# Performance work log

Measured on AMD Instinct MI355X. Metric: run time of the kernel, lower is better.

Reference implementation:

```python
import jax, jax.numpy as jnp
import numpy as np

N_ITER = 30       # fixed-point iterations (repo iterates to tol 3e-6, max 300)
POWER_ITERS = 50  # power iteration steps for spectral radius
KAPPA = 0.9
EPS = 1e-12


def project_l1_ball_rows(W, v):
    # projection_norm_inf: project each row of W onto the L1 ball of radius v
    a = jnp.abs(W)
    s = -jnp.sort(-a, axis=-1)                      # descending |w|
    cs = jnp.cumsum(s, axis=-1)
    k = jnp.arange(1, W.shape[-1] + 1, dtype=W.dtype)
    rho = jnp.sum((s * k > (cs - v)).astype(jnp.int32), axis=-1)  # >= 1
    cs_rho = jnp.take_along_axis(cs, (rho - 1)[:, None], axis=-1)[:, 0]
    theta = (cs_rho - v) / rho.astype(W.dtype)
    proj = jnp.sign(W) * jnp.maximum(a - theta[:, None], 0.0)
    needs = jnp.sum(a, axis=-1) > v
    return jnp.where(needs[:, None], proj, W)


def spmm_XA(X, src, dst, w, n):
    # X @ A with sparse A given as edges A[src, dst] = w ; X: (m, n)
    # (X A)[:, j] = sum_{edges i->j} w * X[:, i]
    return jax.ops.segment_sum(X.T[src] * w[:, None], dst, num_segments=n).T


def spectral_radius(src, dst, w, n):
    v0 = jnp.full((n,), 1.0 / np.sqrt(float(n)), dtype=w.dtype)
    def matvec(v):
        # (A v)[i] = sum_{edges i->j} w * v[j]
        return jax.ops.segment_sum(w * v[dst], src, num_segments=n)
    def body(i, v):
        av = matvec(v)
        return av / (jnp.linalg.norm(av) + EPS)
    v = jax.lax.fori_loop(0, POWER_ITERS, body, v0)
    return jnp.linalg.norm(matvec(v))


def setup_inputs() -> dict:
    key = jax.random.key(0)
    ks = jax.random.split(key, 7)
    n, p, m, c, E = 50000, 256, 128, 40, 800000
    return {
        "features": jax.random.normal(ks[0], (p, n), jnp.float32),
        "W": jax.random.normal(ks[1], (m, m), jnp.float32),
        "Omega_1": jax.random.normal(ks[2], (m, p), jnp.float32),
        "V_w": jax.random.normal(ks[3], (c, m), jnp.float32),
        "X_0": jnp.zeros((m, n), jnp.float32),
        "edge_weight": jax.random.uniform(ks[4], (E,), jnp.float32),
        "edge_src": jax.random.randint(ks[5], (E,), 0, n, jnp.int32),
        "edge_dst": jax.random.randint(ks[6], (E,), 0, n, jnp.int32),
    }


def reference(features, W, Omega_1, V_w, X_0, edge_weight, edge_src, edge_dst):
    n = features.shape[1]
    # spectral radius of A (computed without grad in the original, scipy eigs)
    rho = jax.lax.stop_gradient(spectral_radius(edge_src, edge_dst, edge_weight, n))
    Wp = project_l1_ball_rows(W, KAPPA / rho)
    # b_Omega = Omega_1 @ U @ A  -> (nhid, n)
    b = spmm_XA(Omega_1 @ features, edge_src, edge_dst, edge_weight, n)
    def step(X, _):
        Xn = jax.nn.relu(Wp @ spmm_XA(X, edge_src, edge_dst, edge_weight, n) + b)
        return Xn, None
    X, _ = jax.lax.scan(step, X_0, None, length=N_ITER)
    H = X.T                                        # (n, nhid)
    H = H / jnp.clip(jnp.linalg.norm(H, axis=-1, keepdims=True), EPS)
    # dropout: eval mode -> identity
    return H @ V_w.T                               # (n, nclass)
```

## Files before the change

kernel.cpp:

```cpp
#include <hip/hip_runtime.h>
#include <math.h>

#define N_NODES 50000
#define N_EDGES 800000
#define M_HID   128
#define P_FEAT  256
#define C_OUT   40
#define PWR_ITERS 16
#define FP_ITERS  30
#define KAPPA 0.9f
#define SBLK 256
#define NBK ((N_NODES + 255) / 256)

typedef unsigned short u16;
typedef unsigned int   u32;
typedef __attribute__((ext_vector_type(8))) short short8;
typedef __attribute__((ext_vector_type(4))) float f32x4;

__device__ inline u16 f2bf(float f) {
    union { float f; u32 u; } c; c.f = f;
    u32 u = c.u + 0x7fffu + ((c.u >> 16) & 1u);
    return (u16)(u >> 16);
}
__device__ inline u32 pack2bf(float lo, float hi) {
    return (u32)f2bf(lo) | ((u32)f2bf(hi) << 16);
}
__device__ inline float bflo(u32 u) { union { u32 u; float f; } c; c.u = u << 16; return c.f; }
__device__ inline float bfhi(u32 u) { union { u32 u; float f; } c; c.u = u & 0xffff0000u; return c.f; }


__global__ void fill_pow(float* buf0, float* ss, int n, float val) {
    int i = blockIdx.x * blockDim.x + threadIdx.x;
    if (i < n) buf0[i] = val;
    if (blockIdx.x == 0 && threadIdx.x < 64) ss[threadIdx.x] = (threadIdx.x == 0) ? 1.f : 0.f;
}


__global__ __launch_bounds__(256) void matvec_norm(const int* __restrict__ offs,
                                                   const int2* __restrict__ csr,
                                                   const int* __restrict__ perm,
                                                   const float* __restrict__ vin,
                                                   const float* __restrict__ n2in,
                                                   float* __restrict__ vout,
                                                   float* n2out, int n) {
    int t = blockIdx.x * blockDim.x + threadIdx.x;
    int g = t >> 3, q = t & 7;
    float inv = 1.f / (sqrtf(*n2in) + 1e-12f);
    float a = 0.f;
    int j = -1;
    if (g < n) {
        j = perm[g];
        int lo = offs[j], hi = offs[j + 1];
        for (int e = lo + q; e < hi; e += 8) {
            int2 c = csr[e];
            a += __int_as_float(c.y) * vin[c.x];
        }
    }
    a += __shfl_xor(a, 1, 64);
    a += __shfl_xor(a, 2, 64);
    a += __shfl_xor(a, 4, 64);
    a *= inv;
    if (g < n && q == 0) vout[j] = a;
    float s = (q == 0 && g < n) ? a * a : 0.f;
    for (int o = 32; o > 0; o >>= 1) s += __shfl_down(s, o, 64);
    __shared__ float ls[4];
    int lane = threadIdx.x & 63, wid = threadIdx.x >> 6;
    if (lane == 0) ls[wid] = s;
    __syncthreads();
    if (threadIdx.x == 0) atomicAdd(n2out, ls[0] + ls[1] + ls[2] + ls[3]);
}


__global__ __launch_bounds__(128) void project_w(const float* __restrict__ W,
                                                 const float* __restrict__ rho2,
                                                 u16* __restrict__ Bswz) {
    __shared__ float sa[128];
    __shared__ float ssort[128];
    __shared__ float sc[128];
    __shared__ int cnt2[2];
    int r = blockIdx.x, t = threadIdx.x;
    float radius = KAPPA / sqrtf(*rho2);
    float w0 = W[r * 128 + t];
    float a = fabsf(w0);
    sa[t] = a;
    __syncthreads();
    int rank = 0;
    #pragma unroll 8
    for (int j = 0; j < 128; ++j) {
        float aj = sa[j];
        rank += (aj > a) || (aj == a && j < t);
    }
    ssort[rank] = a;
    __syncthreads();
    sc[t] = ssort[t];
    __syncthreads();
    for (int off = 1; off < 128; off <<= 1) {
        float add = (t >= off) ? sc[t - off] : 0.f;
        __syncthreads();
        sc[t] += add;
        __syncthreads();
    }
    bool flag = ssort[t] * (float)(t + 1) > sc[t] - radius;
    unsigned long long b = __ballot(flag);
    if ((t & 63) == 0) cnt2[t >> 6] = __popcll(b);
    __syncthreads();
    int rho = cnt2[0] + cnt2[1];
    float total = sc[127];
    bool needs = total > radius;
    float theta = (sc[rho - 1] - radius) / (float)rho;
    float o;
    if (needs) {
        float am = a - theta;
        o = (am > 0.f) ? ((w0 > 0.f) ? am : -am) : 0.f;
    } else o = w0;
    int kf = t >> 5, quad = (t >> 3) & 3, jj = t & 7;
    int nt = r >> 4, li = r & 15;
    int l = quad * 16 + li;
    Bswz[((size_t)(kf * 8 + nt) * 64 + l) * 8 + jj] = f2bf(o);
}


__global__ __launch_bounds__(256) void reorder_om(const float* __restrict__ Om,
                                                  u16* __restrict__ Ofrg) {
    int idx = blockIdx.x * 256 + threadIdx.x;
    int r = idx >> 8, k = idx & 255;
    int nt = r >> 4, li = r & 15;
    int kf = k >> 5, sub = (k >> 3) & 3, jj = k & 7;
    int l = sub * 16 + li;
    Ofrg[((size_t)(kf * 8 + nt) * 64 + l) * 8 + jj] = f2bf(Om[idx]);
}


__global__ void count_deg(const int* __restrict__ dst, int* deg, int E) {
    int e = blockIdx.x * blockDim.x + threadIdx.x;
    if (e < E) atomicAdd(&deg[dst[e]], 1);
}

__global__ __launch_bounds__(SBLK) void scan_local(const int* __restrict__ deg,
                                                   int* __restrict__ offsets,
                                                   int* __restrict__ bsum, int n1) {
    __shared__ int s[SBLK];
    int i = blockIdx.x * SBLK + threadIdx.x;
    int v = (i < n1 - 1) ? deg[i] : 0;
    s[threadIdx.x] = v;
    __syncthreads();
    for (int o = 1; o < SBLK; o <<= 1) {
        int add = (threadIdx.x >= o) ? s[threadIdx.x - o] : 0;
        __syncthreads();
        s[threadIdx.x] += add;
        __syncthreads();
    }
    if (i < n1) offsets[i] = s[threadIdx.x] - v;
    if (threadIdx.x == SBLK - 1) bsum[blockIdx.x] = s[SBLK - 1];
}

__global__ __launch_bounds__(SBLK) void scan_bsum(const int* __restrict__ bsum,
                                                  int* __restrict__ bbase, int nb) {
    __shared__ int s[SBLK];
    int v = (threadIdx.x < nb) ? bsum[threadIdx.x] : 0;
    s[threadIdx.x] = v;
    __syncthreads();
    for (int o = 1; o < 256; o <<= 1) {
        int add = (threadIdx.x >= o) ? s[threadIdx.x - o] : 0;
        __syncthreads();
        s[threadIdx.x] += add;
        __syncthreads();
    }
    if (threadIdx.x < nb) bbase[threadIdx.x] = s[threadIdx.x] - v;
}

__global__ __launch_bounds__(SBLK) void scan_add(int* __restrict__ offsets,
                                                 int* __restrict__ cursor,
                                                 const int* __restrict__ bbase, int n1) {
    int i = blockIdx.x * SBLK + threadIdx.x;
    if (i < n1) {
        int o = offsets[i] + bbase[blockIdx.x];
        offsets[i] = o;
        if (i < n1 - 1) cursor[i] = o;
    }
}

__global__ void fill_csr(const int* __restrict__ src, const int* __restrict__ dst,
                         const float* __restrict__ w,
                         int* cur_d, int2* csr_d, int E) {
    int e = blockIdx.x * blockDim.x + threadIdx.x;
    if (e < E) {
        int d = dst[e];
        int pd = atomicAdd(&cur_d[d], 1);
        csr_d[pd] = make_int2(src[e], __float_as_int(w[e]));
    }
}


__global__ __launch_bounds__(256) void bhist(const int* __restrict__ deg,
                                             int* __restrict__ bh, int n) {
    __shared__ int h[256];
    int t = threadIdx.x;
    h[t] = 0;
    __syncthreads();
    int i = blockIdx.x * 256 + t;
    if (i < n) {
        int d = deg[i]; if (d > 255) d = 255;
        atomicAdd(&h[d], 1);
    }
    __syncthreads();
    bh[t * NBK + blockIdx.x] = h[t];
}

__global__ __launch_bounds__(256) void bscatter(const int* __restrict__ deg,
                                                const int* __restrict__ obase,
                                                int* __restrict__ perm, int n) {
    __shared__ int cur[256];
    int t = threadIdx.x;
    cur[t] = obase[t * NBK + blockIdx.x];
    __syncthreads();
    int i = blockIdx.x * 256 + t;
    if (i < n) {
        int d = deg[i]; if (d > 255) d = 255;
        int p = atomicAdd(&cur[d], 1);
        perm[p] = i;
    }
}


__global__ void transpose_x0_bf16(const float* __restrict__ X0, u16* Xb, int n) {
    __shared__ float tile[32][33];
    int jb = blockIdx.x * 32, tb = blockIdx.y * 32;
    int tx = threadIdx.x, ty = threadIdx.y;
    for (int r = 0; r < 32; r += 8) {
        int t = tb + ty + r, j = jb + tx;
        tile[ty + r][tx] = (j < n) ? X0[(size_t)t * n + j] : 0.f;
    }
    __syncthreads();
    for (int r = 0; r < 32; r += 8) {
        int j = jb + ty + r, t = tb + tx;
        if (j < n) Xb[(size_t)j * 128 + t] = f2bf(tile[tx][ty + r]);
    }
}


__global__ __launch_bounds__(256) void gemm_u_mfma(const float* __restrict__ F,
                                                   const u16* __restrict__ Ofrg,
                                                   u16* __restrict__ Utb, int n) {
    __shared__ u32 As32[64][17];
    int tid = threadIdx.x;
    int w = tid >> 6, l = tid & 63;
    int j0 = blockIdx.x * 64;
    const short8* __restrict__ bfr = (const short8*)Ofrg;
    f32x4 acc[8];
    #pragma unroll
    for (int nt = 0; nt < 8; ++nt) acc[nt] = (f32x4){0.f, 0.f, 0.f, 0.f};
    for (int kf = 0; kf < 8; ++kf) {
        int k0 = kf * 32;
        __syncthreads();
        #pragma unroll
        for (int r = 0; r < 4; ++r) {
            int idx = r * 256 + tid;
            int jj = idx & 63, kk2 = idx >> 6;
            int j = j0 + jj;
            float f0 = 0.f, f1 = 0.f;
            if (j < n) {
                f0 = F[(size_t)(k0 + 2 * kk2) * n + j];
                f1 = F[(size_t)(k0 + 2 * kk2 + 1) * n + j];
            }
            As32[jj][kk2] = pack2bf(f0, f1);
        }
        __syncthreads();
        u32 a0 = As32[w * 16 + (l & 15)][(l >> 4) * 4 + 0];
        u32 a1 = As32[w * 16 + (l & 15)][(l >> 4) * 4 + 1];
        u32 a2 = As32[w * 16 + (l & 15)][(l >> 4) * 4 + 2];
        u32 a3 = As32[w * 16 + (l & 15)][(l >> 4) * 4 + 3];
        short8 a;
        a[0] = (short)(a0 & 0xffff); a[1] = (short)(a0 >> 16);
        a[2] = (short)(a1 & 0xffff); a[3] = (short)(a1 >> 16);
        a[4] = (short)(a2 & 0xffff); a[5] = (short)(a2 >> 16);
        a[6] = (short)(a3 & 0xffff); a[7] = (short)(a3 >> 16);
        #pragma unroll
        for (int nt = 0; nt < 8; ++nt) {
            short8 b = bfr[(kf * 8 + nt) * 64 + l];
            acc[nt] = __builtin_amdgcn_mfma_f32_16x16x32_bf16(a, b, acc[nt], 0, 0, 0);
        }
    }
    int rbase = j0 + w * 16 + (l >> 4) * 4;
    int cbase = l & 15;
    #pragma unroll
    for (int nt = 0; nt < 8; ++nt) {
        int col = nt * 16 + cbase;
        #pragma unroll
        for (int i = 0; i < 4; ++i) {
            int row = rbase + i;
            if (row < n) Utb[(size_t)row * 128 + col] = f2bf(acc[nt][i]);
        }
    }
}


__global__ __launch_bounds__(256) void reorder_bt(const u16* __restrict__ btr,
                                                  const int* __restrict__ perm,
                                                  uint2* __restrict__ btf, int n) {
    int t = blockIdx.y * 256 + threadIdx.x;
    int idx16 = blockIdx.x;
    int nt = t >> 6, lane = t & 63;
    int r0 = idx16 * 16 + (lane >> 4) * 4;
    int c = nt * 16 + (lane & 15);
    u16 b0 = (r0 + 0 < n) ? btr[(size_t)perm[r0 + 0] * 128 + c] : 0;
    u16 b1 = (r0 + 1 < n) ? btr[(size_t)perm[r0 + 1] * 128 + c] : 0;
    u16 b2 = (r0 + 2 < n) ? btr[(size_t)perm[r0 + 2] * 128 + c] : 0;
    u16 b3 = (r0 + 3 < n) ? btr[(size_t)perm[r0 + 3] * 128 + c] : 0;
    uint2 o;
    o.x = (u32)b0 | ((u32)b1 << 16);
    o.y = (u32)b2 | ((u32)b3 << 16);
    btf[(size_t)(idx16 * 8 + nt) * 64 + lane] = o;
}


__global__ __launch_bounds__(256) void spmm_bf16(const int* __restrict__ offsets,
                                                 const int2* __restrict__ csr,
                                                 const int* __restrict__ perm,
                                                 const u16* __restrict__ Xin,
                                                 u16* __restrict__ Yout, int n) {
    int tid = threadIdx.x;
    int wid = tid >> 6, lane = tid & 63;
    int q = lane >> 4, li = lane & 15;
    int jp = blockIdx.x * 16 + wid * 4 + q;
    if (jp >= n) return;
    int j = perm[jp];
    int lo = offsets[j], hi = offsets[j + 1];
    const uint4* __restrict__ X4 = (const uint4*)Xin;
    float a[8] = {};
    int e = lo;
    for (; e + 8 <= hi; e += 8) {
        int2 c[8];
        #pragma unroll
        for (int u = 0; u < 8; ++u) c[u] = csr[e + u];
        uint4 x[8];
        #pragma unroll
        for (int u = 0; u < 8; ++u) x[u] = X4[(size_t)c[u].x * 16 + li];
        #pragma unroll
        for (int u = 0; u < 8; ++u) {
            float w = __int_as_float(c[u].y);
            a[0] += w * bflo(x[u].x); a[1] += w * bfhi(x[u].x);
            a[2] += w * bflo(x[u].y); a[3] += w * bfhi(x[u].y);
            a[4] += w * bflo(x[u].z); a[5] += w * bfhi(x[u].z);
            a[6] += w * bflo(x[u].w); a[7] += w * bfhi(x[u].w);
        }
    }
    for (; e < hi; ++e) {
        int2 c = csr[e];
        float w = __int_as_float(c.y);
        uint4 x = X4[(size_t)c.x * 16 + li];
        a[0] += w * bflo(x.x); a[1] += w * bfhi(x.x);
        a[2] += w * bflo(x.y); a[3] += w * bfhi(x.y);
        a[4] += w * bflo(x.z); a[5] += w * bfhi(x.z);
        a[6] += w * bflo(x.w); a[7] += w * bfhi(x.w);
    }
    uint4 o;
    o.x = pack2bf(a[0], a[1]);
    o.y = pack2bf(a[2], a[3]);
    o.z = pack2bf(a[4], a[5]);
    o.w = pack2bf(a[6], a[7]);
    ((uint4*)Yout)[(size_t)j * 16 + li] = o;
}


__global__ __launch_bounds__(512) void fused_fp(const int* __restrict__ offsets,
                                                const int2* __restrict__ csr,
                                                const int* __restrict__ perm,
                                                const u16* __restrict__ Xin,
                                                const u16* __restrict__ Bswz,
                                                const uint2* __restrict__ btf,
                                                u16* __restrict__ Xout, int n) {
    __shared__ uint4 Ys[32][17];
    __shared__ int pj[32];
    int tid = threadIdx.x;

    {
        int qw = tid >> 4, li = tid & 15;
        int jp = blockIdx.x * 32 + qw;
        float a[8] = {};
        if (jp < n) {
            int j = perm[jp];
            if (li == 0) pj[qw] = j;
            int lo = offsets[j], hi = offsets[j + 1];
            const uint4* __restrict__ X4 = (const uint4*)Xin;
            int e = lo;
            for (; e + 8 <= hi; e += 8) {
                int2 c[8];
                #pragma unroll
                for (int u = 0; u < 8; ++u) c[u] = csr[e + u];
                uint4 x[8];
                #pragma unroll
                for (int u = 0; u < 8; ++u) x[u] = X4[(size_t)c[u].x * 16 + li];
                #pragma unroll
                for (int u = 0; u < 8; ++u) {
                    float w = __int_as_float(c[u].y);
                    a[0] += w * bflo(x[u].x); a[1] += w * bfhi(x[u].x);
                    a[2] += w * bflo(x[u].y); a[3] += w * bfhi(x[u].y);
                    a[4] += w * bflo(x[u].z); a[5] += w * bfhi(x[u].z);
                    a[6] += w * bflo(x[u].w); a[7] += w * bfhi(x[u].w);
                }
            }
            for (; e < hi; ++e) {
                int2 c = csr[e];
                float w = __int_as_float(c.y);
                uint4 x = X4[(size_t)c.x * 16 + li];
                a[0] += w * bflo(x.x); a[1] += w * bfhi(x.x);
                a[2] += w * bflo(x.y); a[3] += w * bfhi(x.y);
                a[4] += w * bflo(x.z); a[5] += w * bfhi(x.z);
                a[6] += w * bflo(x.w); a[7] += w * bfhi(x.w);
            }
        }
        uint4 o;
        o.x = pack2bf(a[0], a[1]);
        o.y = pack2bf(a[2], a[3]);
        o.z = pack2bf(a[4], a[5]);
        o.w = pack2bf(a[6], a[7]);
        Ys[qw][li] = o;
    }
    __syncthreads();

    int w = tid >> 6, l = tid & 63;
    int rg = w & 1;
    int ntb = (w >> 1) * 2;
    f32x4 acc[2];
    acc[0] = (f32x4){0.f, 0.f, 0.f, 0.f};
    acc[1] = (f32x4){0.f, 0.f, 0.f, 0.f};
    const short8* __restrict__ bfr = (const short8*)Bswz;
    #pragma unroll
    for (int kf = 0; kf < 4; ++kf) {
        short8 a = *((const short8*)&Ys[rg * 16 + (l & 15)][kf * 4 + (l >> 4)]);
        #pragma unroll
        for (int t = 0; t < 2; ++t) {
            short8 b = bfr[(kf * 8 + ntb + t) * 64 + l];
            acc[t] = __builtin_amdgcn_mfma_f32_16x16x32_bf16(a, b, acc[t], 0, 0, 0);
        }
    }
    int pidx16 = blockIdx.x * 2 + rg;
    int lrbase = rg * 16 + (l >> 4) * 4;
    int cbase = l & 15;
    #pragma unroll
    for (int t = 0; t < 2; ++t) {
        int nt = ntb + t;
        uint2 bb = btf[(size_t)(pidx16 * 8 + nt) * 64 + l];
        float bi[4] = {bflo(bb.x), bfhi(bb.x), bflo(bb.y), bfhi(bb.y)};
        int col = nt * 16 + cbase;
        #pragma unroll
        for (int i = 0; i < 4; ++i) {
            int jp = blockIdx.x * 32 + lrbase + i;
            if (jp < n) {
                int j = pj[lrbase + i];
                float v = acc[t][i] + bi[i];
                Xout[(size_t)j * 128 + col] = f2bf(v > 0.f ? v : 0.f);
            }
        }
    }
}


__global__ __launch_bounds__(256) void final_out(const u16* __restrict__ Xb,
                                                 const float* __restrict__ Vw,
                                                 float* __restrict__ out, int n) {
    __shared__ float Vs[40][132];
    int tid = threadIdx.x;
    int jb = blockIdx.x * 64;
    for (int i = tid; i < 40 * 128; i += 256) {
        int c = i >> 7, k = i & 127;
        Vs[c][(k >> 5) * 33 + (k & 31)] = Vw[i];
    }
    int g = tid >> 2, q = tid & 3;
    int j = jb + g;
    float xs[32];
    float ssq = 0.f;
    if (j < n) {
        const uint4* X4 = (const uint4*)(Xb + (size_t)j * 128) + q * 4;
        #pragma unroll
        for (int v = 0; v < 4; ++v) {
            uint4 u = X4[v];
            xs[v * 8 + 0] = bflo(u.x); xs[v * 8 + 1] = bfhi(u.x);
            xs[v * 8 + 2] = bflo(u.y); xs[v * 8 + 3] = bfhi(u.y);
            xs[v * 8 + 4] = bflo(u.z); xs[v * 8 + 5] = bfhi(u.z);
            xs[v * 8 + 6] = bflo(u.w); xs[v * 8 + 7] = bfhi(u.w);
        }
        #pragma unroll
        for (int m = 0; m < 32; ++m) ssq += xs[m] * xs[m];
    } else {
        #pragma unroll
        for (int m = 0; m < 32; ++m) xs[m] = 0.f;
    }
    ssq += __shfl_xor(ssq, 1, 64);
    ssq += __shfl_xor(ssq, 2, 64);
    float inv = 1.f / fmaxf(sqrtf(ssq), 1e-12f);
    #pragma unroll
    for (int m = 0; m < 32; ++m) xs[m] *= inv;
    __syncthreads();
    float pacc[10];
    #pragma unroll
    for (int cc = 0; cc < 10; ++cc) pacc[cc] = 0.f;
    #pragma unroll 1
    for (int c = 0; c < 40; ++c) {
        const float* vrow = &Vs[c][q * 33];
        float acc = 0.f;
        #pragma unroll
        for (int m = 0; m < 32; ++m) acc += xs[m] * vrow[m];
        acc += __shfl_xor(acc, 1, 64);
        acc += __shfl_xor(acc, 2, 64);
        if ((c & 3) == q) pacc[c >> 2] = acc;
    }
    if (j < n) {
        #pragma unroll
        for (int cc = 0; cc < 10; ++cc) {
            int c = cc * 4 + q;
            out[(size_t)j * 40 + c] = pacc[cc];
        }
    }
}


extern "C" void kernel_launch(void* const* d_in, const int* in_sizes, int n_in,
                              void* d_out, int out_size, void* d_ws, size_t ws_size,
                              hipStream_t stream) {
    const float* F    = (const float*)d_in[0];
    const float* W    = (const float*)d_in[1];
    const float* Om   = (const float*)d_in[2];
    const float* Vw   = (const float*)d_in[3];
    const float* X0   = (const float*)d_in[4];
    const float* ew   = (const float*)d_in[5];
    const int*   esrc = (const int*)d_in[6];
    const int*   edst = (const int*)d_in[7];
    float* out = (float*)d_out;
    (void)in_sizes; (void)n_in; (void)out_size; (void)ws_size;

    char* ws = (char*)d_ws;
    size_t off = 0;
    auto alloc = [&](size_t bytes) -> void* {
        void* p = ws + off;
        off = (off + bytes + 255) & ~(size_t)255;
        return p;
    };
    float* buf0    = (float*)alloc((size_t)N_NODES * 4);
    float* buf1    = (float*)alloc((size_t)N_NODES * 4);
    float* ss      = (float*)alloc(64 * 4);
    int*   deg     = (int*)  alloc((size_t)(N_NODES + 1) * 4);
    int*   offs_d  = (int*)  alloc((size_t)(N_NODES + 1) * 4);
    int*   cur_d   = (int*)  alloc((size_t)N_NODES * 4);
    int*   bsum    = (int*)  alloc(512 * 4);
    int*   bbase   = (int*)  alloc(512 * 4);
    int*   bh      = (int*)  alloc((size_t)(256 * NBK + 1) * 4);
    int*   obase   = (int*)  alloc((size_t)(256 * NBK + 1) * 4);
    int*   ocur    = (int*)  alloc((size_t)(256 * NBK + 1) * 4);
    int*   perm    = (int*)  alloc((size_t)N_NODES * 4);
    int2*  csr_d   = (int2*) alloc((size_t)N_EDGES * 8);
    u16*   Bswz    = (u16*)  alloc(128 * 128 * 2);
    u16*   Ofrg    = (u16*)  alloc(128 * 256 * 2);
    u16*   btr     = (u16*)  alloc((size_t)N_NODES * 128 * 2);
    uint2* btf     = (uint2*)alloc((size_t)3200 * 512 * 8);
    u16*   Utb     = (u16*)  alloc((size_t)N_NODES * 128 * 2);
    u16*   Xa      = (u16*)  alloc((size_t)N_NODES * 128 * 2);
    u16*   Xb      = (u16*)  alloc((size_t)N_NODES * 128 * 2);

    hipMemsetAsync(deg, 0, (size_t)(N_NODES + 1) * 4, stream);

    const int n1 = N_NODES + 1;
    const int nb = (n1 + SBLK - 1) / SBLK;

    count_deg<<<(N_EDGES + 255) / 256, 256, 0, stream>>>(edst, deg, N_EDGES);
    scan_local<<<nb, SBLK, 0, stream>>>(deg, offs_d, bsum, n1);
    scan_bsum<<<1, SBLK, 0, stream>>>(bsum, bbase, nb);
    scan_add<<<nb, SBLK, 0, stream>>>(offs_d, cur_d, bbase, n1);
    fill_csr<<<(N_EDGES + 255) / 256, 256, 0, stream>>>(
        esrc, edst, ew, cur_d, csr_d, N_EDGES);

    bhist<<<NBK, 256, 0, stream>>>(deg, bh, N_NODES);
    {
        const int sn1 = 256 * NBK + 1;
        const int snb = (sn1 + SBLK - 1) / SBLK;
        scan_local<<<snb, SBLK, 0, stream>>>(bh, obase, bsum, sn1);
        scan_bsum<<<1, SBLK, 0, stream>>>(bsum, bbase, snb);
        scan_add<<<snb, SBLK, 0, stream>>>(obase, ocur, bbase, sn1);
    }
    bscatter<<<NBK, 256, 0, stream>>>(deg, obase, perm, N_NODES);

    fill_pow<<<(N_NODES + 255) / 256, 256, 0, stream>>>(
        buf0, ss, N_NODES, 1.f / sqrtf((float)N_NODES));
    float* bufs[2] = {buf0, buf1};
    for (int it = 0; it <= PWR_ITERS; ++it) {
        matvec_norm<<<(8 * N_NODES + 255) / 256, 256, 0, stream>>>(
            offs_d, csr_d, perm, bufs[it & 1], ss + it,
            bufs[(it + 1) & 1], ss + it + 1, N_NODES);
    }

    project_w<<<128, 128, 0, stream>>>(W, ss + PWR_ITERS + 1, Bswz);

    reorder_om<<<128, 256, 0, stream>>>(Om, Ofrg);
    gemm_u_mfma<<<(N_NODES + 63) / 64, 256, 0, stream>>>(F, Ofrg, Utb, N_NODES);
    spmm_bf16<<<(N_NODES + 15) / 16, 256, 0, stream>>>(offs_d, csr_d, perm, Utb, btr, N_NODES);
    reorder_bt<<<dim3((N_NODES + 15) / 16, 2), 256, 0, stream>>>(btr, perm, btf, N_NODES);

    transpose_x0_bf16<<<dim3((N_NODES + 31) / 32, 4), dim3(32, 8), 0, stream>>>(X0, Xa, N_NODES);
    u16* xb2[2] = {Xa, Xb};
    for (int it = 0; it < FP_ITERS; ++it) {
        fused_fp<<<(N_NODES + 31) / 32, 512, 0, stream>>>(
            offs_d, csr_d, perm, xb2[it & 1], Bswz, btf, xb2[(it + 1) & 1], N_NODES);
    }

    final_out<<<(N_NODES + 63) / 64, 256, 0, stream>>>(xb2[FP_ITERS & 1], Vw, out, N_NODES);
}
```

Measured before the change: 1.946 ms.

## Store fixed-point iterate in degree-permuted order and fuse power iteration cooperatively

Node rows of the fixed-point iterate are now kept in the degree-sorted permuted order. An inverse permutation remaps the CSR column indices, and the permutation is applied only when X0 is loaded and when the final output is written. This makes the row writes in each fused_fp iteration contiguous and removes the per-block shared permutation lookup. Separately, the 17 power-iteration launches are replaced by one cooperative kernel that uses grid.sync between steps, removing launch gaps. The cost is a one-time remap kernel and extra buffers, plus a dependence on all 1563 cooperative blocks being resident at once.

```diff
diff --git a/kernel.cpp b/kernel.cpp
--- a/kernel.cpp
+++ b/kernel.cpp
@@ -1,5 +1,8 @@
 #include <hip/hip_runtime.h>
+#include <hip/hip_cooperative_groups.h>
 #include <math.h>
+
+namespace cg = cooperative_groups;
 
 #define N_NODES 50000
 #define N_EDGES 800000
@@ -36,38 +39,45 @@
 }
 
 
-__global__ __launch_bounds__(256) void matvec_norm(const int* __restrict__ offs,
-                                                   const int2* __restrict__ csr,
-                                                   const int* __restrict__ perm,
-                                                   const float* __restrict__ vin,
-                                                   const float* __restrict__ n2in,
-                                                   float* __restrict__ vout,
-                                                   float* n2out, int n) {
+__global__ __launch_bounds__(256) void power_coop(const int* __restrict__ offs,
+                                                  const int2* __restrict__ csr,
+                                                  const int* __restrict__ perm,
+                                                  float* buf0, float* buf1,
+                                                  float* ss, int n) {
+    cg::grid_group grid = cg::this_grid();
     int t = blockIdx.x * blockDim.x + threadIdx.x;
     int g = t >> 3, q = t & 7;
-    float inv = 1.f / (sqrtf(*n2in) + 1e-12f);
-    float a = 0.f;
-    int j = -1;
+    int j = -1, lo = 0, hi = 0;
     if (g < n) {
         j = perm[g];
-        int lo = offs[j], hi = offs[j + 1];
-        for (int e = lo + q; e < hi; e += 8) {
-            int2 c = csr[e];
-            a += __int_as_float(c.y) * vin[c.x];
-        }
-    }
-    a += __shfl_xor(a, 1, 64);
-    a += __shfl_xor(a, 2, 64);
-    a += __shfl_xor(a, 4, 64);
-    a *= inv;
-    if (g < n && q == 0) vout[j] = a;
-    float s = (q == 0 && g < n) ? a * a : 0.f;
-    for (int o = 32; o > 0; o >>= 1) s += __shfl_down(s, o, 64);
+        lo = offs[j]; hi = offs[j + 1];
+    }
     __shared__ float ls[4];
     int lane = threadIdx.x & 63, wid = threadIdx.x >> 6;
-    if (lane == 0) ls[wid] = s;
-    __syncthreads();
-    if (threadIdx.x == 0) atomicAdd(n2out, ls[0] + ls[1] + ls[2] + ls[3]);
+    float* bufs[2] = {buf0, buf1};
+    for (int it = 0; it <= PWR_ITERS; ++it) {
+        const float* __restrict__ vin = bufs[it & 1];
+        float* __restrict__ vout = bufs[(it + 1) & 1];
+        float inv = 1.f / (sqrtf(ss[it]) + 1e-12f);
+        float a = 0.f;
+        if (g < n) {
+            for (int e = lo + q; e < hi; e += 8) {
+                int2 c = csr[e];
+                a += __int_as_float(c.y) * vin[c.x];
+            }
+        }
+        a += __shfl_xor(a, 1, 64);
+        a += __shfl_xor(a, 2, 64);
+        a += __shfl_xor(a, 4, 64);
+        a *= inv;
+        if (g < n && q == 0) vout[j] = a;
+        float s = (q == 0 && g < n) ? a * a : 0.f;
+        for (int o = 32; o > 0; o >>= 1) s += __shfl_down(s, o, 64);
+        if (lane == 0) ls[wid] = s;
+        __syncthreads();
+        if (threadIdx.x == 0) atomicAdd(&ss[it + 1], ls[0] + ls[1] + ls[2] + ls[3]);
+        grid.sync();
+    }
 }
 
 
@@ -222,8 +232,24 @@
     }
 }
 
-
-__global__ void transpose_x0_bf16(const float* __restrict__ X0, u16* Xb, int n) {
+__global__ void build_invperm(const int* __restrict__ perm, int* __restrict__ invp, int n) {
+    int i = blockIdx.x * blockDim.x + threadIdx.x;
+    if (i < n) invp[perm[i]] = i;
+}
+
+__global__ void remap_csr(const int2* __restrict__ in, const int* __restrict__ invp,
+                          int2* __restrict__ outp, int E) {
+    int e = blockIdx.x * blockDim.x + threadIdx.x;
+    if (e < E) {
+        int2 c = in[e];
+        c.x = invp[c.x];
+        outp[e] = c;
+    }
+}
+
+
+__global__ void transpose_x0_bf16(const float* __restrict__ X0, const int* __restrict__ invp,
+                                  u16* Xb, int n) {
     __shared__ float tile[32][33];
     int jb = blockIdx.x * 32, tb = blockIdx.y * 32;
     int tx = threadIdx.x, ty = threadIdx.y;
@@ -234,7 +260,7 @@
     __syncthreads();
     for (int r = 0; r < 32; r += 8) {
         int j = jb + ty + r, t = tb + tx;
-        if (j < n) Xb[(size_t)j * 128 + t] = f2bf(tile[tx][ty + r]);
+        if (j < n) Xb[(size_t)invp[j] * 128 + t] = f2bf(tile[tx][ty + r]);
     }
 }
 
@@ -364,14 +390,13 @@
 
 
 __global__ __launch_bounds__(512) void fused_fp(const int* __restrict__ offsets,
-                                                const int2* __restrict__ csr,
+                                                const int2* __restrict__ csrp,
                                                 const int* __restrict__ perm,
                                                 const u16* __restrict__ Xin,
                                                 const u16* __restrict__ Bswz,
                                                 const uint2* __restrict__ btf,
                                                 u16* __restrict__ Xout, int n) {
     __shared__ uint4 Ys[32][17];
-    __shared__ int pj[32];
     int tid = threadIdx.x;
 
     {
@@ -380,14 +405,13 @@
         float a[8] = {};
         if (jp < n) {
             int j = perm[jp];
-            if (li == 0) pj[qw] = j;
             int lo = offsets[j], hi = offsets[j + 1];
             const uint4* __restrict__ X4 = (const uint4*)Xin;
             int e = lo;
             for (; e + 8 <= hi; e += 8) {
                 int2 c[8];
                 #pragma unroll
-                for (int u = 0; u < 8; ++u) c[u] = csr[e + u];
+                for (int u = 0; u < 8; ++u) c[u] = csrp[e + u];
                 uint4 x[8];
                 #pragma unroll
                 for (int u = 0; u < 8; ++u) x[u] = X4[(size_t)c[u].x * 16 + li];
@@ -401,7 +425,7 @@
                 }
             }
             for (; e < hi; ++e) {
-                int2 c = csr[e];
+                int2 c = csrp[e];
                 float w = __int_as_float(c.y);
                 uint4 x = X4[(size_t)c.x * 16 + li];
                 a[0] += w * bflo(x.x); a[1] += w * bfhi(x.x);
@@ -448,9 +472,8 @@
         for (int i = 0; i < 4; ++i) {
             int jp = blockIdx.x * 32 + lrbase + i;
             if (jp < n) {
-                int j = pj[lrbase + i];
                 float v = acc[t][i] + bi[i];
-                Xout[(size_t)j * 128 + col] = f2bf(v > 0.f ? v : 0.f);
+                Xout[(size_t)jp * 128 + col] = f2bf(v > 0.f ? v : 0.f);
             }
         }
     }
@@ -458,6 +481,7 @@
 
 
 __global__ __launch_bounds__(256) void final_out(const u16* __restrict__ Xb,
+                                                 const int* __restrict__ perm,
                                                  const float* __restrict__ Vw,
                                                  float* __restrict__ out, int n) {
     __shared__ float Vs[40][132];
@@ -468,11 +492,11 @@
         Vs[c][(k >> 5) * 33 + (k & 31)] = Vw[i];
     }
     int g = tid >> 2, q = tid & 3;
-    int j = jb + g;
+    int jp = jb + g;
     float xs[32];
     float ssq = 0.f;
-    if (j < n) {
-        const uint4* X4 = (const uint4*)(Xb + (size_t)j * 128) + q * 4;
+    if (jp < n) {
+        const uint4* X4 = (const uint4*)(Xb + (size_t)jp * 128) + q * 4;
         #pragma unroll
         for (int v = 0; v < 4; ++v) {
             uint4 u = X4[v];
@@ -506,7 +530,8 @@
         acc += __shfl_xor(acc, 2, 64);
         if ((c & 3) == q) pacc[c >> 2] = acc;
     }
-    if (j < n) {
+    if (jp < n) {
+        int j = perm[jp];
         #pragma unroll
         for (int cc = 0; cc < 10; ++cc) {
             int c = cc * 4 + q;
@@ -549,7 +574,9 @@
     int*   obase   = (int*)  alloc((size_t)(256 * NBK + 1) * 4);
     int*   ocur    = (int*)  alloc((size_t)(256 * NBK + 1) * 4);
     int*   perm    = (int*)  alloc((size_t)N_NODES * 4);
+    int*   invp    = (int*)  alloc((size_t)N_NODES * 4);
     int2*  csr_d   = (int2*) alloc((size_t)N_EDGES * 8);
+    int2*  csrp    = (int2*) alloc((size_t)N_EDGES * 8);
     u16*   Bswz    = (u16*)  alloc(128 * 128 * 2);
     u16*   Ofrg    = (u16*)  alloc(128 * 256 * 2);
     u16*   btr     = (u16*)  alloc((size_t)N_NODES * 128 * 2);
@@ -579,14 +606,18 @@
         scan_add<<<snb, SBLK, 0, stream>>>(obase, ocur, bbase, sn1);
     }
     bscatter<<<NBK, 256, 0, stream>>>(deg, obase, perm, N_NODES);
+    build_invperm<<<(N_NODES + 255) / 256, 256, 0, stream>>>(perm, invp, N_NODES);
+    remap_csr<<<(N_EDGES + 255) / 256, 256, 0, stream>>>(csr_d, invp, csrp, N_EDGES);
 
     fill_pow<<<(N_NODES + 255) / 256, 256, 0, stream>>>(
         buf0, ss, N_NODES, 1.f / sqrtf((float)N_NODES));
-    float* bufs[2] = {buf0, buf1};
-    for (int it = 0; it <= PWR_ITERS; ++it) {
-        matvec_norm<<<(8 * N_NODES + 255) / 256, 256, 0, stream>>>(
-            offs_d, csr_d, perm, bufs[it & 1], ss + it,
-            bufs[(it + 1) & 1], ss + it + 1, N_NODES);
+    {
+        int n_arg = N_NODES;
+        void* args[] = {(void*)&offs_d, (void*)&csr_d, (void*)&perm,
+                        (void*)&buf0, (void*)&buf1, (void*)&ss, (void*)&n_arg};
+        hipLaunchCooperativeKernel((void*)power_coop,
+                                   dim3((8 * N_NODES + 255) / 256), dim3(256),
+                                   args, 0, stream);
     }
 
     project_w<<<128, 128, 0, stream>>>(W, ss + PWR_ITERS + 1, Bswz);
@@ -596,12 +627,12 @@
     spmm_bf16<<<(N_NODES + 15) / 16, 256, 0, stream>>>(offs_d, csr_d, perm, Utb, btr, N_NODES);
     reorder_bt<<<dim3((N_NODES + 15) / 16, 2), 256, 0, stream>>>(btr, perm, btf, N_NODES);
 
-    transpose_x0_bf16<<<dim3((N_NODES + 31) / 32, 4), dim3(32, 8), 0, stream>>>(X0, Xa, N_NODES);
+    transpose_x0_bf16<<<dim3((N_NODES + 31) / 32, 4), dim3(32, 8), 0, stream>>>(X0, invp, Xa, N_NODES);
     u16* xb2[2] = {Xa, Xb};
     for (int it = 0; it < FP_ITERS; ++it) {
         fused_fp<<<(N_NODES + 31) / 32, 512, 0, stream>>>(
-            offs_d, csr_d, perm, xb2[it & 1], Bswz, btf, xb2[(it + 1) & 1], N_NODES);
-    }
-
-    final_out<<<(N_NODES + 63) / 64, 256, 0, stream>>>(xb2[FP_ITERS & 1], Vw, out, N_NODES);
-}
+            offs_d, csrp, perm, xb2[it & 1], Bswz, btf, xb2[(it + 1) & 1], N_NODES);
+    }
+
+    final_out<<<(N_NODES + 63) / 64, 256, 0, stream>>>(xb2[FP_ITERS & 1], perm, Vw, out, N_NODES);
+}
```

Measured after the change: 4.614 ms. +137.1%, slower.
